# Kernel tuning notes

Measured on AMD Instinct MI355X. Metric: run time of the kernel, lower is better.

Reference implementation:

```python
import jax, jax.numpy as jnp
import numpy as np

N, E, FD, PD, C0, C1 = 50000, 1000000, 1024, 64, 64, 64


def setup_inputs() -> dict:
    key = jax.random.key(0)
    ks = iter(jax.random.split(key, 64))
    nrm = lambda s, sc=0.05: jax.random.normal(next(ks), s, jnp.float32) * sc

    def bn_p(c):
        # rows: gamma, beta, running_mean, running_var (eval-mode batchnorm)
        return jnp.stack([
            1.0 + 0.1 * jax.random.normal(next(ks), (c,)),
            0.1 * jax.random.normal(next(ks), (c,)),
            0.1 * jax.random.normal(next(ks), (c,)),
            0.5 + jax.random.uniform(next(ks), (c,)),
        ]).astype(jnp.float32)

    inp = {}
    inp["x"] = jax.random.normal(next(ks), (N, FD + 4), jnp.float32)
    inp["edge_index"] = jax.random.randint(next(ks), (2, E), 0, N, jnp.int32)
    inp["edge_attr"] = jax.random.randint(next(ks), (E,), 0, 3, jnp.int32) - 1  # {-1,0,1}
    inp["Wspf"] = nrm((PD, 4)); inp["bspf"] = nrm((PD,))
    inp["W011"] = nrm((C0, FD // 2 + PD)); inp["b011"] = nrm((C0,))
    inp["W012"] = nrm((C0, FD // 2)); inp["b012"] = nrm((C0,))
    inp["bn01"] = bn_p(C0)
    for i in (1, 2, 3):
        inp[f"e{i}W1"] = nrm((C0, 2 * C0)); inp[f"e{i}b1"] = nrm((C0,))
        inp[f"e{i}W2"] = nrm((C0, C0)); inp[f"e{i}b2"] = nrm((C0,))
        inp[f"bn1{i}"] = bn_p(C0)
    inp["s21Wl"] = nrm((C1, C0)); inp["s21bl"] = nrm((C1,)); inp["s21Wr"] = nrm((C1, C0))
    inp["bn21"] = bn_p(C1)
    for i in (1, 2, 3):
        inp[f"s3{i}Wl"] = nrm((1, C1)); inp[f"s3{i}bl"] = nrm((1,)); inp[f"s3{i}Wr"] = nrm((1, C1))
    return inp


def _bn(h, p):
    g, b, m, v = p
    return (h - m) * jax.lax.rsqrt(v + 1e-5) * g + b


def _edge_conv(h, src, dst, seg, n, W1, b1, W2, b2):
    # EdgeConv: max_j MLP([x_i, x_j - x_i]); masked edges routed to dummy segment n
    xi, xj = h[dst], h[src]
    msg = jax.nn.relu(jnp.concatenate([xi, xj - xi], axis=1) @ W1.T + b1) @ W2.T + b2
    out = jax.ops.segment_max(msg, seg, num_segments=n + 1)[:n]
    return jnp.where(jnp.isfinite(out), out, 0.0)  # nodes with no in-edges -> 0


def _sage(h, src, seg, n, Wl, bl, Wr):
    # SAGEConv: lin_l(mean_j x_j) + lin_r(x_i)
    s = jax.ops.segment_sum(h[src], seg, num_segments=n + 1)[:n]
    cnt = jax.ops.segment_sum(jnp.ones((seg.shape[0],), h.dtype), seg, num_segments=n + 1)[:n]
    agg = s / jnp.maximum(cnt, 1.0)[:, None]
    return agg @ Wl.T + bl + h @ Wr.T


def reference(x, edge_index, edge_attr, Wspf, bspf, W011, b011, W012, b012, bn01,
              e1W1, e1b1, e1W2, e1b2, bn11, e2W1, e2b1, e2W2, e2b2, bn12,
              e3W1, e3b1, e3W2, e3b2, bn13, s21Wl, s21bl, s21Wr, bn21,
              s31Wl, s31bl, s31Wr, s32Wl, s32bl, s32Wr, s33Wl, s33bl, s33Wr):
    fd = 1024
    n = x.shape[0]
    src, dst = edge_index[0], edge_index[1]
    seg1 = jnp.where(edge_attr >= 0, dst, n)  # forward-time edges
    seg2 = jnp.where(edge_attr <= 0, dst, n)  # backward-time edges
    seg3 = dst                                 # all edges

    spf = x[:, fd:fd + 4]
    x_vis = jnp.concatenate([x[:, fd // 2:fd], spf @ Wspf.T + bspf], axis=1) @ W011.T + b011
    x_aud = x[:, :fd // 2] @ W012.T + b012
    h = jax.nn.relu(_bn(x_aud + x_vis, bn01))

    def branch(eW1, eb1, eW2, eb2, bnE, seg, sWl, sbl, sWr):
        y = jax.nn.relu(_bn(_edge_conv(h, src, dst, seg, n, eW1, eb1, eW2, eb2), bnE))
        y = jax.nn.relu(_bn(_sage(y, src, seg, n, s21Wl, s21bl, s21Wr), bn21))
        return _sage(y, src, seg, n, sWl, sbl, sWr)

    o = (branch(e1W1, e1b1, e1W2, e1b2, bn11, seg1, s31Wl, s31bl, s31Wr)
         + branch(e2W1, e2b1, e2W2, e2b2, bn12, seg2, s32Wl, s32bl, s32Wr)
         + branch(e3W1, e3b1, e3W2, e3b2, bn13, seg3, s33Wl, s33bl, s33Wr))
    return jax.nn.sigmoid(o)
```

## Files before the change

### kernel.cpp

```cpp
#include <hip/hip_runtime.h>
#include <cstdint>
#include <cstddef>

#define NN 50000
#define EE 1000000
#define NBK 196
#define PWAVES 5120

typedef __attribute__((ext_vector_type(8))) short bf16x8;
typedef __attribute__((ext_vector_type(4))) short s16x4;
typedef __attribute__((ext_vector_type(4))) float f32x4;
typedef _Float16 f16;
typedef __attribute__((ext_vector_type(2))) _Float16 f16x2;
typedef __attribute__((ext_vector_type(4))) _Float16 f16x4;
typedef __attribute__((ext_vector_type(8))) _Float16 f16x8;

__device__ __forceinline__ unsigned short f2bf(float f) {
    union { unsigned int i; float f; } v; v.f = f;
    unsigned int u = v.i;
    u = u + 0x7FFFu + ((u >> 16) & 1u);
    return (unsigned short)(u >> 16);
}

__device__ __forceinline__ void split2(float v, short& hi, short& lo) {
    union { float f; unsigned int u; } a; a.f = v;
    unsigned short h16 = (unsigned short)(a.u >> 16);
    union { unsigned int u; float f; } hf; hf.u = ((unsigned int)h16) << 16;
    union { float f; unsigned int u; } b; b.f = v - hf.f;
    hi = (short)h16;
    lo = (short)(b.u >> 16);
}

#define OFF_WHL    ((size_t)0)
#define OFF_WSPP   ((size_t)262144)
#define OFF_BIAS01 ((size_t)263168)
#define OFF_W1PQT  ((size_t)263424)
#define OFF_BIASPQ ((size_t)361728)
#define OFF_WSAGET ((size_t)363264)
#define OFF_BIAS21 ((size_t)396032)
#define OFF_BNF    ((size_t)396288)
#define OFF_W2BF   ((size_t)398848)
#define OFF_INVC4  ((size_t)423424)
#define OFF_PZ4    ((size_t)1223424)
#define OFF_RP     ((size_t)2023424)
#define OFF_PARTS  ((size_t)2223488)
#define OFF_DEG    ((size_t)2227584)
#define OFF_GHEAD  ((size_t)2427648)
#define OFF_SORT   ((size_t)2431744)
#define OFF_H      ((size_t)6431744)
#define OFF_PI     ((size_t)19231744)
#define OFF_QI     ((size_t)38431744)
#define OFF_Y1I    ((size_t)57631744)
#define OFF_EBUCK  OFF_H
#define OFF_AGGI   OFF_PI

__global__ __launch_bounds__(256) void k_prep(
    const float* __restrict__ Wspf, const float* __restrict__ bspf,
    const float* __restrict__ W011, const float* __restrict__ b011,
    const float* __restrict__ W012, const float* __restrict__ b012,
    const float* __restrict__ bn01,
    const float* __restrict__ e1W1, const float* __restrict__ e1b1,
    const float* __restrict__ e1b2, const float* __restrict__ bn11,
    const float* __restrict__ e2W1, const float* __restrict__ e2b1,
    const float* __restrict__ e2b2, const float* __restrict__ bn12,
    const float* __restrict__ e3W1, const float* __restrict__ e3b1,
    const float* __restrict__ e3b2, const float* __restrict__ bn13,
    const float* __restrict__ e1W2, const float* __restrict__ e2W2,
    const float* __restrict__ e3W2,
    const float* __restrict__ s21Wl, const float* __restrict__ s21bl,
    const float* __restrict__ s21Wr, const float* __restrict__ bn21,
    unsigned short* __restrict__ Whl, float* __restrict__ WspP, float* __restrict__ bias01,
    float* __restrict__ W1pqT, float* __restrict__ biasPQ,
    float* __restrict__ WsageT, float* __restrict__ bias21, float* __restrict__ bnf,
    f16* __restrict__ W2h)
{
    int idx = blockIdx.x * 256 + threadIdx.x;
    if (idx < 131072) {
        int hl = idx >> 16;
        int r = idx & 65535;
        int kchunk = r >> 11;
        int r2 = r & 2047;
        int blk = r2 >> 9;
        int r3 = r2 & 511;
        int lane = r3 >> 3;
        int j = r3 & 7;
        int n = lane & 15, quad = lane >> 4;
        int k = kchunk * 32 + quad * 8 + j;
        int c = blk * 16 + n;
        float s = bn01[c] * rsqrtf(bn01[192 + c] + 1e-5f);
        float w = ((k < 512) ? W012[c * 512 + k] : W011[c * 576 + (k - 512)]) * s;
        short hi, lo;
        split2(w, hi, lo);
        Whl[idx] = (unsigned short)(hl ? lo : hi);
    } else if (idx < 131072 + 24576) {
        int r = idx - 131072;
        int b = r >> 13; r &= 8191;
        int k = r >> 7, cp = r & 127;
        const float* W1 = (b == 0) ? e1W1 : (b == 1) ? e2W1 : e3W1;
        float val;
        if (cp < 64) val = W1[cp * 128 + k] - W1[cp * 128 + 64 + k];
        else         val = W1[(cp - 64) * 128 + 64 + k];
        W1pqT[b * 8192 + k * 128 + cp] = val;
    } else if (idx < 131072 + 24576 + 8192) {
        int r = idx - (131072 + 24576);
        int k = r >> 6, c = r & 63;
        float s = bn21[c] * rsqrtf(bn21[192 + c] + 1e-5f);
        float w = (k < 64) ? s21Wl[c * 64 + k] : s21Wr[c * 64 + (k - 64)];
        WsageT[k * 64 + c] = w * s;
    } else if (idx < 131072 + 24576 + 8192 + 64) {
        int c = idx - (131072 + 24576 + 8192);
        float s01 = bn01[c] * rsqrtf(bn01[192 + c] + 1e-5f);
        float wsp0 = 0.f, wsp1 = 0.f, wsp2 = 0.f, wsp3 = 0.f, bacc = 0.f;
        for (int j = 0; j < 64; j++) {
            float w = W011[c * 576 + 512 + j];
            wsp0 += w * Wspf[j * 4 + 0];
            wsp1 += w * Wspf[j * 4 + 1];
            wsp2 += w * Wspf[j * 4 + 2];
            wsp3 += w * Wspf[j * 4 + 3];
            bacc += w * bspf[j];
        }
        WspP[c * 4 + 0] = wsp0 * s01; WspP[c * 4 + 1] = wsp1 * s01;
        WspP[c * 4 + 2] = wsp2 * s01; WspP[c * 4 + 3] = wsp3 * s01;
        bias01[c] = (b011[c] + b012[c] + bacc) * s01 + (bn01[64 + c] - bn01[128 + c] * s01);
        float s21 = bn21[c] * rsqrtf(bn21[192 + c] + 1e-5f);
        bias21[c] = s21bl[c] * s21 + (bn21[64 + c] - bn21[128 + c] * s21);
        const float* b1a[3] = { e1b1, e2b1, e3b1 };
        const float* b2a[3] = { e1b2, e2b2, e3b2 };
        const float* bna[3] = { bn11, bn12, bn13 };
#pragma unroll
        for (int b = 0; b < 3; b++) {
            float s = bna[b][c] * rsqrtf(bna[b][192 + c] + 1e-5f);
            float tr = bna[b][64 + c] - bna[b][128 + c] * s;
            bnf[b * 192 + c] = s;
            bnf[b * 192 + 64 + c] = b2a[b][c] * s + tr;
            bnf[b * 192 + 128 + c] = tr;
            biasPQ[b * 128 + c] = b1a[b][c];
            biasPQ[b * 128 + 64 + c] = 0.f;
        }
    } else if (idx < 131072 + 24576 + 8192 + 64 + 12288) {
        int r = idx - (131072 + 24576 + 8192 + 64);
        int b = r >> 12, i = r & 4095;
        const float* W2 = (b == 0) ? e1W2 : (b == 1) ? e2W2 : e3W2;
        W2h[b * 4096 + i] = (f16)W2[i];
    }
}

__global__ __launch_bounds__(256) void k_hist(
    const int* __restrict__ dst, int* __restrict__ deg)
{
    int e = blockIdx.x * 256 + threadIdx.x;
    if (e < EE) atomicAdd(&deg[dst[e]], 1);
}

__global__ __launch_bounds__(256) void k_psum(const int* __restrict__ deg, int* __restrict__ parts)
{
    int i = blockIdx.x * 256 + threadIdx.x;
    int v = (i < NN) ? deg[i] : 0;
#pragma unroll
    for (int off = 32; off > 0; off >>= 1) v += __shfl_xor(v, off);
    __shared__ int ws4[4];
    int wid = threadIdx.x >> 6;
    if ((threadIdx.x & 63) == 0) ws4[wid] = v;
    __syncthreads();
    if (threadIdx.x == 0)
        parts[blockIdx.x] = ws4[0] + ws4[1] + ws4[2] + ws4[3];
}

__global__ __launch_bounds__(256) void k_pscan(int* __restrict__ parts)
{
    __shared__ int sbuf[256];
    int tid = threadIdx.x;
    int v = (tid < NBK) ? parts[tid] : 0;
    sbuf[tid] = v;
    __syncthreads();
    for (int off = 1; off < 256; off <<= 1) {
        int t = (tid >= off) ? sbuf[tid - off] : 0;
        __syncthreads();
        sbuf[tid] += t;
        __syncthreads();
    }
    if (tid < NBK) parts[tid] = sbuf[tid] - v;
}

__global__ __launch_bounds__(256) void k_scanfix(
    const int* __restrict__ deg, const int* __restrict__ parts, int* __restrict__ rowptr)
{
    __shared__ int sbuf[256];
    int tid = threadIdx.x;
    int i = blockIdx.x * 256 + tid;
    int v = (i < NN) ? deg[i] : 0;
    sbuf[tid] = v;
    __syncthreads();
    for (int off = 1; off < 256; off <<= 1) {
        int t = (tid >= off) ? sbuf[tid - off] : 0;
        __syncthreads();
        sbuf[tid] += t;
        __syncthreads();
    }
    int base = parts[blockIdx.x];
    if (i < NN)      rowptr[i] = base + sbuf[tid] - v;
    if (i == NN - 1) rowptr[NN] = base + sbuf[tid];
}

__global__ __launch_bounds__(256) void k_gheadinit(
    const int* __restrict__ rp, int* __restrict__ ghead)
{
    int t = threadIdx.x;
    if (t < NBK) ghead[t] = rp[t * 256];
}

__global__ __launch_bounds__(256) void k_bucketA(
    const int* __restrict__ src, const int* __restrict__ dst, const int* __restrict__ attr,
    int* __restrict__ ghead, unsigned int* __restrict__ ebuck)
{
    __shared__ int hist[NBK];
    __shared__ int head[NBK];
    int tid = threadIdx.x;
    if (tid < NBK) hist[tid] = 0;
    __syncthreads();
    int base_e = blockIdx.x * 4096;
    unsigned int word[16]; int bkt[16];
#pragma unroll
    for (int k = 0; k < 16; k++) {
        int e = base_e + k * 256 + tid;
        if (e < EE) {
            int d = dst[e], s = src[e], a = attr[e] + 1;
            int b = d >> 8;
            word[k] = (unsigned)s | ((unsigned)a << 16) | ((unsigned)(d & 255) << 18);
            bkt[k] = b;
            atomicAdd(&hist[b], 1);
        } else { bkt[k] = -1; word[k] = 0; }
    }
    __syncthreads();
    if (tid < NBK) {
        int c = hist[tid];
        head[tid] = c ? atomicAdd(&ghead[tid], c) : 0;
    }
    __syncthreads();
#pragma unroll
    for (int k = 0; k < 16; k++) {
        if (bkt[k] >= 0) {
            int pos = atomicAdd(&head[bkt[k]], 1);
            ebuck[pos] = word[k];
        }
    }
}

__global__ __launch_bounds__(256) void k_bucketB(
    const int* __restrict__ rp, const unsigned int* __restrict__ ebuck,
    int* __restrict__ sorted)
{
    __shared__ int sbuf[256];
    __shared__ int head[256];
    int b = blockIdx.x, tid = threadIdx.x;
    int n0 = b * 256;
    int n1 = n0 + 256; if (n1 > NN) n1 = NN;
    int r0 = rp[n0];
    int r1 = rp[n1];
    sbuf[tid] = 0;
    __syncthreads();
    for (int e = r0 + tid; e < r1; e += 256)
        atomicAdd(&sbuf[(ebuck[e] >> 18) & 255], 1);
    __syncthreads();
    int v = sbuf[tid];
    for (int off = 1; off < 256; off <<= 1) {
        int t = (tid >= off) ? sbuf[tid - off] : 0;
        __syncthreads();
        sbuf[tid] += t;
        __syncthreads();
    }
    head[tid] = r0 + sbuf[tid] - v;
    __syncthreads();
    for (int e = r0 + tid; e < r1; e += 256) {
        unsigned int w = ebuck[e];
        int pos = atomicAdd(&head[(w >> 18) & 255], 1);
        sorted[pos] = (int)(w & 0x3FFFFu);
    }
}

__global__ __launch_bounds__(256) void k_h(
    const float* __restrict__ x, const unsigned short* __restrict__ Whl,
    const float* __restrict__ WspP, const float* __restrict__ bias01,
    float* __restrict__ h)
{
    __shared__ unsigned short hib[2][4096];
    __shared__ unsigned short lob[2][4096];
    int tid = threadIdx.x;
    int w = tid >> 6, l = tid & 63;
    int tile = blockIdx.x;
    int m = l & 15, quad = l >> 4;
    int blk = w;
    const unsigned short* Wh = Whl;
    const unsigned short* Wl = Whl + 65536;
    const size_t xbase = (size_t)tile * 16 * 1028;

    int oct_w = l >> 1, off_w = (l & 1) * 4;

    f32x4 g[4];
#pragma unroll
    for (int p = 0; p < 4; p++)
        g[p] = *(const f32x4*)(x + xbase + (size_t)(p * 4 + w) * 1028 + l * 4);
#pragma unroll
    for (int p = 0; p < 4; p++) {
        int r = p * 4 + w;
        int op = r * 256 + (oct_w ^ (r & 7)) * 8 + off_w;
        s16x4 h4, l4;
#pragma unroll
        for (int i = 0; i < 4; i++) { short hi, lo; split2(g[p][i], hi, lo); h4[i] = hi; l4[i] = lo; }
        *(s16x4*)(&hib[0][op]) = h4;
        *(s16x4*)(&lob[0][op]) = l4;
    }
    __syncthreads();

    f32x4 acc = { 0.f, 0.f, 0.f, 0.f };
    for (int c = 0; c < 4; c++) {
        if (c < 3) {
#pragma unroll
            for (int p = 0; p < 4; p++)
                g[p] = *(const f32x4*)(x + xbase + (size_t)(p * 4 + w) * 1028 + (c + 1) * 256 + l * 4);
        }
        int buf = c & 1;
        const unsigned short* hp = &hib[buf][m * 256];
        const unsigned short* lp = &lob[buf][m * 256];
        int msw = m & 7;
#pragma unroll
        for (int ks = 0; ks < 8; ks++) {
            int oct = ks * 4 + quad;
            int ao = (oct ^ msw) * 8;
            bf16x8 xh = *(const bf16x8*)(hp + ao);
            bf16x8 xl = *(const bf16x8*)(lp + ao);
            int fb = (c * 8 + ks) * 2048 + blk * 512 + l * 8;
            bf16x8 bh = *(const bf16x8*)(Wh + fb);
            bf16x8 bl = *(const bf16x8*)(Wl + fb);
            acc = __builtin_amdgcn_mfma_f32_16x16x32_bf16(xh, bh, acc, 0, 0, 0);
            acc = __builtin_amdgcn_mfma_f32_16x16x32_bf16(xl, bh, acc, 0, 0, 0);
            acc = __builtin_amdgcn_mfma_f32_16x16x32_bf16(xh, bl, acc, 0, 0, 0);
        }
        if (c < 3) {
            int nbuf = (c + 1) & 1;
#pragma unroll
            for (int p = 0; p < 4; p++) {
                int r = p * 4 + w;
                int op = r * 256 + (oct_w ^ (r & 7)) * 8 + off_w;
                s16x4 h4, l4;
#pragma unroll
                for (int i = 0; i < 4; i++) { short hi, lo; split2(g[p][i], hi, lo); h4[i] = hi; l4[i] = lo; }
                *(s16x4*)(&hib[nbuf][op]) = h4;
                *(s16x4*)(&lob[nbuf][op]) = l4;
            }
            __syncthreads();
        }
    }

    int ch = blk * 16 + m;
    f32x4 wsp = *(const f32x4*)(WspP + ch * 4);
    float bia = bias01[ch];
#pragma unroll
    for (int r = 0; r < 4; r++) {
        int row = tile * 16 + quad * 4 + r;
        f32x4 sp = *(const f32x4*)(x + (size_t)row * 1028 + 1024);
        float a = acc[r] + sp[0] * wsp[0] + sp[1] * wsp[1]
                + sp[2] * wsp[2] + sp[3] * wsp[3] + bia;
        h[(size_t)row * 64 + ch] = fmaxf(a, 0.f);
    }
}

__global__ __launch_bounds__(256) void k_pq(
    const float* __restrict__ h, const float* __restrict__ WT,
    const float* __restrict__ biasP, f16* __restrict__ Pi, f16* __restrict__ Qi)
{
    __shared__ float wt[64 * 128];
    __shared__ float xt[64 * 68];
    int tid = threadIdx.x;
    int m0 = blockIdx.x * 64;
    int cg = tid & 31, rg = tid >> 5;
#pragma unroll
    for (int i = 0; i < 8; i++)
        ((float4*)wt)[i * 256 + tid] = ((const float4*)WT)[i * 256 + tid];
#pragma unroll
    for (int i = 0; i < 4; i++) {
        int li = i * 256 + tid;
        int rr = li >> 4, q = li & 15;
        int row = m0 + rr;
        float4 u = make_float4(0.f, 0.f, 0.f, 0.f);
        if (row < NN) u = *(const float4*)(h + (size_t)row * 64 + q * 4);
        *(float4*)(xt + rr * 68 + q * 4) = u;
    }
    __syncthreads();
    float acc[8][4];
#pragma unroll
    for (int r = 0; r < 8; r++)
#pragma unroll
        for (int j = 0; j < 4; j++) acc[r][j] = 0.f;
#pragma unroll 8
    for (int k = 0; k < 64; k++) {
        float4 wv = *(const float4*)(wt + k * 128 + cg * 4);
#pragma unroll
        for (int r = 0; r < 8; r++) {
            float xv = xt[(rg * 8 + r) * 68 + k];
            acc[r][0] += xv * wv.x; acc[r][1] += xv * wv.y;
            acc[r][2] += xv * wv.z; acc[r][3] += xv * wv.w;
        }
    }
#pragma unroll
    for (int r = 0; r < 8; r++) {
        int row = m0 + rg * 8 + r;
        if (row < NN) {
            if (cg < 16) {
                f16x4 res;
#pragma unroll
                for (int j = 0; j < 4; j++)
                    res[j] = (f16)(acc[r][j] + biasP[cg * 4 + j]);
                *(f16x4*)(Pi + (size_t)row * 192 + cg * 4) = res;
            } else {
                f16x4 res;
#pragma unroll
                for (int j = 0; j < 4; j++)
                    res[j] = (f16)acc[r][j];
                *(f16x4*)(Qi + (size_t)row * 192 + (cg - 16) * 4) = res;
            }
        }
    }
}

#define ECV_LDS_BRANCH(B, PL, PH, Q0, Q1, MASK, ACC)                               \
    if ((MASK) & 0xFFFFull) {                                                      \
        f16x8 a0, a1;                                                              \
        _Pragma("unroll") for (int j = 0; j < 8; j++) {                            \
            f16 s0 = PL[j] + Q0[j]; a0[j] = (s0 > (f16)0.f) ? s0 : (f16)0.f;       \
            f16 s1 = PH[j] + Q1[j]; a1[j] = (s1 > (f16)0.f) ? s1 : (f16)0.f;       \
        }                                                                          \
        _Pragma("unroll") for (int blk = 0; blk < 4; blk++) {                      \
            f32x4 c = { 0.f, 0.f, 0.f, 0.f };                                      \
            f16x8 w0 = *(const f16x8*)(w2s + ((B) * 8 + blk * 2 + 0) * 512 + quad * 128 + m * 8); \
            f16x8 w1 = *(const f16x8*)(w2s + ((B) * 8 + blk * 2 + 1) * 512 + quad * 128 + m * 8); \
            c = __builtin_amdgcn_mfma_f32_16x16x32_f16(a0, w0, c, 0, 0, 0);        \
            c = __builtin_amdgcn_mfma_f32_16x16x32_f16(a1, w1, c, 0, 0, 0);        \
            _Pragma("unroll") for (int r = 0; r < 4; r++)                          \
                if (((MASK) >> (vsh + r)) & 1)                                     \
                    ACC[blk][r] = fmaxf(ACC[blk][r], c[r]);                        \
        }                                                                          \
    }

#define ECV_EPI(B, ACC, CNT)                                                       \
    {                                                                              \
        float red[4];                                                              \
        _Pragma("unroll") for (int blk = 0; blk < 4; blk++) {                      \
            float rv = fmaxf(fmaxf(ACC[blk][0], ACC[blk][1]),                      \
                             fmaxf(ACC[blk][2], ACC[blk][3]));                     \
            rv = fmaxf(rv, __shfl_xor(rv, 16));                                    \
            rv = fmaxf(rv, __shfl_xor(rv, 32));                                    \
            red[blk] = rv;                                                         \
        }                                                                          \
        float mx = red[quad];                                                      \
        const float* scb = bnf + (B) * 192;                                        \
        float outv = ((CNT) > 0) ? fmaxf(fmaf(mx, scb[lane], scb[64 + lane]), 0.f) \
                                 : fmaxf(scb[128 + lane], 0.f);                    \
        y1i[(size_t)v * 192 + (B) * 64 + lane] = (f16)outv;                        \
    }

__global__ __launch_bounds__(256) void k_edgeconv_f(
    const int* __restrict__ rowptr, const int* __restrict__ sorted,
    const f16* __restrict__ Pi, const f16* __restrict__ Qi,
    const f16* __restrict__ W2h,
    const float* __restrict__ bnf,
    f16* __restrict__ y1i, float* __restrict__ invc4)
{
    __shared__ f16 w2s[8192];
    int tid = threadIdx.x;
#pragma unroll
    for (int u0 = 0; u0 < 4; u0++) {
        int u = u0 * 256 + tid;
        int frag = u >> 6;
        int rem = u & 63;
        int m2 = rem >> 2, qd = rem & 3;
        int bb = frag >> 3, blk = (frag >> 1) & 3, kc = frag & 1;
        *(int4*)(w2s + frag * 512 + qd * 128 + m2 * 8) =
            *(const int4*)(W2h + (bb * 64 + blk * 16 + m2) * 64 + kc * 32 + qd * 8);
    }
    __syncthreads();

    int wid = tid >> 6, lane = tid & 63;
    int m = lane & 15, quad = lane >> 4;
    int gw = blockIdx.x * 4 + wid;

    f16x8 wf3[4][2];
#pragma unroll
    for (int blk = 0; blk < 4; blk++)
#pragma unroll
        for (int kc = 0; kc < 2; kc++)
            wf3[blk][kc] = *(const f16x8*)(W2h + 2 * 4096 + (blk * 16 + m) * 64 + kc * 32 + quad * 8);

    for (int v = gw; v < NN; v += PWAVES) {
        const f16* pr = Pi + (size_t)v * 192;
        f16x8 pl0 = *(const f16x8*)(pr + 0   + quad * 8);
        f16x8 ph0 = *(const f16x8*)(pr + 32  + quad * 8);
        f16x8 pl1 = *(const f16x8*)(pr + 64  + quad * 8);
        f16x8 ph1 = *(const f16x8*)(pr + 96  + quad * 8);
        f16x8 pl2 = *(const f16x8*)(pr + 128 + quad * 8);
        f16x8 ph2 = *(const f16x8*)(pr + 160 + quad * 8);

        int e0 = rowptr[v], e1 = rowptr[v + 1];
        int deg = e1 - e0;
        float acc0[4][4], acc1[4][4], acc2[4][4];
#pragma unroll
        for (int blk = 0; blk < 4; blk++)
#pragma unroll
            for (int r = 0; r < 4; r++) {
                acc0[blk][r] = -3.0e38f; acc1[blk][r] = -3.0e38f; acc2[blk][r] = -3.0e38f;
            }

        int cnt1 = 0, cnt2 = 0;
        int nb = (deg + 15) >> 4;
        for (int bi = 0; bi < nb; bi++) {
            int e = e0 + bi * 16 + m;
            bool in = e < e1;
            int wrd = in ? sorted[e] : 0;
            int srcm = in ? (wrd & 0xFFFF) : v;
            int a = (wrd >> 16) & 3;
            bool mm1 = in && (a >= 1);
            bool mm2 = in && (a <= 1);
            const f16* qr = Qi + (size_t)srcm * 192;
            f16x8 q30 = *(const f16x8*)(qr + 128 + quad * 8);
            f16x8 q31 = *(const f16x8*)(qr + 160 + quad * 8);
            f16x8 q10 = {}, q11 = {}, q20 = {}, q21 = {};
            if (mm1) { q10 = *(const f16x8*)(qr + quad * 8);      q11 = *(const f16x8*)(qr + 32 + quad * 8); }
            if (mm2) { q20 = *(const f16x8*)(qr + 64 + quad * 8); q21 = *(const f16x8*)(qr + 96 + quad * 8); }
            unsigned long long bl1 = __ballot(mm1);
            unsigned long long bl2 = __ballot(mm2);
            unsigned long long bl3 = __ballot(in);
            cnt1 += __popc((unsigned)bl1 & 0xFFFFu);
            cnt2 += __popc((unsigned)bl2 & 0xFFFFu);
            int vsh = quad * 4;

            {
                f16x8 a0, a1;
#pragma unroll
                for (int j = 0; j < 8; j++) {
                    f16 s0 = pl2[j] + q30[j]; a0[j] = (s0 > (f16)0.f) ? s0 : (f16)0.f;
                    f16 s1 = ph2[j] + q31[j]; a1[j] = (s1 > (f16)0.f) ? s1 : (f16)0.f;
                }
#pragma unroll
                for (int blk = 0; blk < 4; blk++) {
                    f32x4 c = { 0.f, 0.f, 0.f, 0.f };
                    c = __builtin_amdgcn_mfma_f32_16x16x32_f16(a0, wf3[blk][0], c, 0, 0, 0);
                    c = __builtin_amdgcn_mfma_f32_16x16x32_f16(a1, wf3[blk][1], c, 0, 0, 0);
#pragma unroll
                    for (int r = 0; r < 4; r++)
                        if ((bl3 >> (vsh + r)) & 1)
                            acc2[blk][r] = fmaxf(acc2[blk][r], c[r]);
                }
            }
            ECV_LDS_BRANCH(0, pl0, ph0, q10, q11, bl1, acc0)
            ECV_LDS_BRANCH(1, pl1, ph1, q20, q21, bl2, acc1)
        }

        ECV_EPI(0, acc0, cnt1)
        ECV_EPI(1, acc1, cnt2)
        ECV_EPI(2, acc2, deg)
        if (lane == 0) {
            float4 ic;
            ic.x = 1.f / (float)(cnt1 > 0 ? cnt1 : 1);
            ic.y = 1.f / (float)(cnt2 > 0 ? cnt2 : 1);
            ic.z = 1.f / (float)(deg  > 0 ? deg  : 1);
            ic.w = 0.f;
            *(float4*)(invc4 + (size_t)v * 4) = ic;
        }
    }
}

__global__ __launch_bounds__(256) void k_agg_f(
    const int* __restrict__ rowptr, const int* __restrict__ sorted,
    const f16* __restrict__ y1i, const float* __restrict__ invc4,
    f16* __restrict__ aggi)
{
    int wid = threadIdx.x >> 6, lane = threadIdx.x & 63;
    int hf = lane >> 5, c = lane & 31;
    int gw = blockIdx.x * 4 + wid;
    for (int v = gw; v < NN; v += PWAVES) {
        int e0 = rowptr[v], e1 = rowptr[v + 1];
        float s1a = 0.f, s1b = 0.f, s2a = 0.f, s2b = 0.f, s3a = 0.f, s3b = 0.f;
        float t1a = 0.f, t1b = 0.f, t2a = 0.f, t2b = 0.f, t3a = 0.f, t3b = 0.f;
        int e = e0;
        for (; e + 4 <= e1; e += 4) {
            int wA = sorted[e + hf];
            int wB = sorted[e + 2 + hf];
            {
                int src = wA & 0xFFFF, a = (wA >> 16) & 3;
                const f16* row = y1i + (size_t)src * 192 + c * 2;
                f16x2 u3 = *(const f16x2*)(row + 128); s3a += (float)u3[0]; s3b += (float)u3[1];
                if (a >= 1) { f16x2 u = *(const f16x2*)(row);      s1a += (float)u[0]; s1b += (float)u[1]; }
                if (a <= 1) { f16x2 u = *(const f16x2*)(row + 64); s2a += (float)u[0]; s2b += (float)u[1]; }
            }
            {
                int src = wB & 0xFFFF, a = (wB >> 16) & 3;
                const f16* row = y1i + (size_t)src * 192 + c * 2;
                f16x2 u3 = *(const f16x2*)(row + 128); t3a += (float)u3[0]; t3b += (float)u3[1];
                if (a >= 1) { f16x2 u = *(const f16x2*)(row);      t1a += (float)u[0]; t1b += (float)u[1]; }
                if (a <= 1) { f16x2 u = *(const f16x2*)(row + 64); t2a += (float)u[0]; t2b += (float)u[1]; }
            }
        }
        for (; e + 2 <= e1; e += 2) {
            int wA = sorted[e + hf];
            int src = wA & 0xFFFF, a = (wA >> 16) & 3;
            const f16* row = y1i + (size_t)src * 192 + c * 2;
            f16x2 u3 = *(const f16x2*)(row + 128); s3a += (float)u3[0]; s3b += (float)u3[1];
            if (a >= 1) { f16x2 u = *(const f16x2*)(row);      s1a += (float)u[0]; s1b += (float)u[1]; }
            if (a <= 1) { f16x2 u = *(const f16x2*)(row + 64); s2a += (float)u[0]; s2b += (float)u[1]; }
        }
        if (e < e1 && hf == 0) {
            int wA = sorted[e];
            int src = wA & 0xFFFF, a = (wA >> 16) & 3;
            const f16* row = y1i + (size_t)src * 192 + c * 2;
            f16x2 u3 = *(const f16x2*)(row + 128); s3a += (float)u3[0]; s3b += (float)u3[1];
            if (a >= 1) { f16x2 u = *(const f16x2*)(row);      s1a += (float)u[0]; s1b += (float)u[1]; }
            if (a <= 1) { f16x2 u = *(const f16x2*)(row + 64); s2a += (float)u[0]; s2b += (float)u[1]; }
        }
        s1a += t1a; s1b += t1b; s2a += t2a; s2b += t2b; s3a += t3a; s3b += t3b;
        s1a += __shfl_xor(s1a, 32); s1b += __shfl_xor(s1b, 32);
        s2a += __shfl_xor(s2a, 32); s2b += __shfl_xor(s2b, 32);
        s3a += __shfl_xor(s3a, 32); s3b += __shfl_xor(s3b, 32);
        if (hf == 0) {
            float4 icv = *(const float4*)(invc4 + (size_t)v * 4);
            f16* od = aggi + (size_t)v * 192 + c * 2;
            f16x2 r1; r1[0] = (f16)(s1a * icv.x); r1[1] = (f16)(s1b * icv.x); *(f16x2*)(od)       = r1;
            f16x2 r2; r2[0] = (f16)(s2a * icv.y); r2[1] = (f16)(s2b * icv.y); *(f16x2*)(od + 64)  = r2;
            f16x2 r3; r3[0] = (f16)(s3a * icv.z); r3[1] = (f16)(s3b * icv.z); *(f16x2*)(od + 128) = r3;
        }
    }
}

__global__ __launch_bounds__(256) void k_sage1(
    const f16* __restrict__ aggA, const f16* __restrict__ y1A,
    const float* __restrict__ WsageT, const float* __restrict__ bias21,
    const float* __restrict__ Wl3, const float* __restrict__ bl3,
    const float* __restrict__ Wr3,
    float* __restrict__ pz4, int b)
{
    __shared__ float wt[64 * 64];
    __shared__ float xt[128 * 68];
    __shared__ float wl[64], wr[64];
    int tid = threadIdx.x;
    int m0 = blockIdx.x * 128;
    int cg = tid & 15, rg = tid >> 4;
    if (tid < 64) { wl[tid] = Wl3[tid]; wr[tid] = Wr3[tid]; }
    float blv = bl3[0];
    float acc[8][4];
#pragma unroll
    for (int r = 0; r < 8; r++)
#pragma unroll
        for (int j = 0; j < 4; j++) acc[r][j] = 0.f;
    for (int ch = 0; ch < 2; ch++) {
        const f16* A = ch ? y1A : aggA;
        __syncthreads();
#pragma unroll
        for (int i = 0; i < 4; i++)
            ((float4*)wt)[i * 256 + tid] = ((const float4*)(WsageT + ch * 4096))[i * 256 + tid];
#pragma unroll
        for (int i = 0; i < 4; i++) {
            int li = i * 256 + tid;
            int rr = li >> 3, q = li & 7;
            int row = m0 + rr;
            f16x8 u = {};
            if (row < NN) u = *(const f16x8*)(A + (size_t)row * 192 + q * 8);
            float4 lo4 = make_float4((float)u[0], (float)u[1], (float)u[2], (float)u[3]);
            float4 hi4 = make_float4((float)u[4], (float)u[5], (float)u[6], (float)u[7]);
            *(float4*)(xt + rr * 68 + q * 8) = lo4;
            *(float4*)(xt + rr * 68 + q * 8 + 4) = hi4;
        }
        __syncthreads();
#pragma unroll 8
        for (int k = 0; k < 64; k++) {
            float4 wv = *(const float4*)(wt + k * 64 + cg * 4);
#pragma unroll
            for (int r = 0; r < 8; r++) {
                float xv = xt[(rg * 8 + r) * 68 + k];
                acc[r][0] += xv * wv.x; acc[r][1] += xv * wv.y;
                acc[r][2] += xv * wv.z; acc[r][3] += xv * wv.w;
            }
        }
    }
#pragma unroll
    for (int r = 0; r < 8; r++) {
        int row = m0 + rg * 8 + r;
        float ap = 0.f, az = 0.f;
#pragma unroll
        for (int j = 0; j < 4; j++) {
            float t = fmaxf(acc[r][j] + bias21[cg * 4 + j], 0.f);
            ap += t * wl[cg * 4 + j];
            az += t * wr[cg * 4 + j];
        }
        ap += __shfl_xor(ap, 1); ap += __shfl_xor(ap, 2);
        ap += __shfl_xor(ap, 4); ap += __shfl_xor(ap, 8);
        az += __shfl_xor(az, 1); az += __shfl_xor(az, 2);
        az += __shfl_xor(az, 4); az += __shfl_xor(az, 8);
        if (cg == 0 && row < NN) {
            pz4[(size_t)row * 4 + b] = ap;
            float zz = az + blv;
            if (b == 0) pz4[(size_t)row * 4 + 3] = zz;
            else        pz4[(size_t)row * 4 + 3] += zz;
        }
    }
}

__global__ __launch_bounds__(256) void k_sage2_f(
    const int* __restrict__ rowptr, const int* __restrict__ sorted,
    const float* __restrict__ pz4, const float* __restrict__ invc4,
    float* __restrict__ outp)
{
    int wid = threadIdx.x >> 6, lane = threadIdx.x & 63;
    int gw = blockIdx.x * 4 + wid;
    for (int v = gw; v < NN; v += PWAVES) {
        int e0 = rowptr[v], e1 = rowptr[v + 1];
        float s1 = 0.f, s2 = 0.f, s3 = 0.f;
        for (int e = e0 + lane; e < e1; e += 64) {
            int w = sorted[e];
            int src = w & 0xFFFF, a = (w >> 16) & 3;
            float4 pz = *(const float4*)(pz4 + (size_t)src * 4);
            s3 += pz.z;
            if (a >= 1) s1 += pz.x;
            if (a <= 1) s2 += pz.y;
        }
#pragma unroll
        for (int off = 32; off > 0; off >>= 1) {
            s1 += __shfl_xor(s1, off);
            s2 += __shfl_xor(s2, off);
            s3 += __shfl_xor(s3, off);
        }
        if (lane == 0) {
            float4 icv = *(const float4*)(invc4 + (size_t)v * 4);
            float zsum = pz4[(size_t)v * 4 + 3];
            float val = s1 * icv.x + s2 * icv.y + s3 * icv.z + zsum;
            outp[v] = 1.f / (1.f + expf(-val));
        }
    }
}

extern "C" void kernel_launch(void* const* d_in, const int* in_sizes, int n_in,
                              void* d_out, int out_size, void* d_ws, size_t ws_size,
                              hipStream_t stream)
{
    const float* x    = (const float*)d_in[0];
    const int* ei     = (const int*)d_in[1];
    const int* attr   = (const int*)d_in[2];
    const float* Wspf = (const float*)d_in[3];
    const float* bspf = (const float*)d_in[4];
    const float* W011 = (const float*)d_in[5];
    const float* b011 = (const float*)d_in[6];
    const float* W012 = (const float*)d_in[7];
    const float* b012 = (const float*)d_in[8];
    const float* bn01 = (const float*)d_in[9];
    const float* eW1[3] = { (const float*)d_in[10], (const float*)d_in[15], (const float*)d_in[20] };
    const float* eb1[3] = { (const float*)d_in[11], (const float*)d_in[16], (const float*)d_in[21] };
    const float* eW2[3] = { (const float*)d_in[12], (const float*)d_in[17], (const float*)d_in[22] };
    const float* eb2[3] = { (const float*)d_in[13], (const float*)d_in[18], (const float*)d_in[23] };
    const float* bn1[3] = { (const float*)d_in[14], (const float*)d_in[19], (const float*)d_in[24] };
    const float* s21Wl = (const float*)d_in[25];
    const float* s21bl = (const float*)d_in[26];
    const float* s21Wr = (const float*)d_in[27];
    const float* bn21  = (const float*)d_in[28];
    const float* s3Wl[3] = { (const float*)d_in[29], (const float*)d_in[32], (const float*)d_in[35] };
    const float* s3bl[3] = { (const float*)d_in[30], (const float*)d_in[33], (const float*)d_in[36] };
    const float* s3Wr[3] = { (const float*)d_in[31], (const float*)d_in[34], (const float*)d_in[37] };

    char* ws = (char*)d_ws;
    unsigned short* Whl = (unsigned short*)(ws + OFF_WHL);
    float* WspP   = (float*)(ws + OFF_WSPP);
    float* bias01 = (float*)(ws + OFF_BIAS01);
    float* W1pqT  = (float*)(ws + OFF_W1PQT);
    float* biasPQ = (float*)(ws + OFF_BIASPQ);
    float* WsageT = (float*)(ws + OFF_WSAGET);
    float* bias21 = (float*)(ws + OFF_BIAS21);
    float* bnf    = (float*)(ws + OFF_BNF);
    f16*   W2h    = (f16*)(ws + OFF_W2BF);
    float* invc4  = (float*)(ws + OFF_INVC4);
    float* pz4    = (float*)(ws + OFF_PZ4);
    int*   rp     = (int*)(ws + OFF_RP);
    int*   parts  = (int*)(ws + OFF_PARTS);
    int*   deg    = (int*)(ws + OFF_DEG);
    int*   ghead  = (int*)(ws + OFF_GHEAD);
    int*   sorted = (int*)(ws + OFF_SORT);
    unsigned int* ebuck = (unsigned int*)(ws + OFF_EBUCK);
    float* h      = (float*)(ws + OFF_H);
    f16*   Pi     = (f16*)(ws + OFF_PI);
    f16*   Qi     = (f16*)(ws + OFF_QI);
    f16*   y1i    = (f16*)(ws + OFF_Y1I);
    f16*   aggi   = (f16*)(ws + OFF_AGGI);

    hipMemsetAsync(ws + OFF_DEG, 0, 200064, stream);

    k_prep<<<689, 256, 0, stream>>>(
        Wspf, bspf, W011, b011, W012, b012, bn01,
        eW1[0], eb1[0], eb2[0], bn1[0],
        eW1[1], eb1[1], eb2[1], bn1[1],
        eW1[2], eb1[2], eb2[2], bn1[2],
        eW2[0], eW2[1], eW2[2],
        s21Wl, s21bl, s21Wr, bn21,
        Whl, WspP, bias01, W1pqT, biasPQ, WsageT, bias21, bnf, W2h);

    k_hist<<<3907, 256, 0, stream>>>(ei + EE, deg);
    k_psum<<<NBK, 256, 0, stream>>>(deg, parts);
    k_pscan<<<1, 256, 0, stream>>>(parts);
    k_scanfix<<<NBK, 256, 0, stream>>>(deg, parts, rp);
    k_gheadinit<<<1, 256, 0, stream>>>(rp, ghead);
    k_bucketA<<<245, 256, 0, stream>>>(ei, ei + EE, attr, ghead, ebuck);
    k_bucketB<<<NBK, 256, 0, stream>>>(rp, ebuck, sorted);

    k_h<<<3125, 256, 0, stream>>>(x, Whl, WspP, bias01, h);

    for (int b = 0; b < 3; b++)
        k_pq<<<782, 256, 0, stream>>>(h, W1pqT + b * 8192, biasPQ + b * 128,
                                      Pi + b * 64, Qi + b * 64);

    k_edgeconv_f<<<PWAVES / 4, 256, 0, stream>>>(rp, sorted, Pi, Qi, W2h, bnf, y1i, invc4);
    k_agg_f<<<PWAVES / 4, 256, 0, stream>>>(rp, sorted, y1i, invc4, aggi);

    for (int b = 0; b < 3; b++)
        k_sage1<<<391, 256, 0, stream>>>(aggi + b * 64, y1i + b * 64, WsageT, bias21,
                                         s3Wl[b], s3bl[b], s3Wr[b], pz4, b);

    k_sage2_f<<<PWAVES / 4, 256, 0, stream>>>(rp, sorted, pz4, invc4, (float*)d_out);
}
```

Baseline: 846.5 us.

## Merge PQ launches, split edgeconv full/tail blocks, widen agg gathers

```diff
diff --git a/kernel.cpp b/kernel.cpp
--- a/kernel.cpp
+++ b/kernel.cpp
@@ -15,13 +15,6 @@
 typedef __attribute__((ext_vector_type(4))) _Float16 f16x4;
 typedef __attribute__((ext_vector_type(8))) _Float16 f16x8;
 
-__device__ __forceinline__ unsigned short f2bf(float f) {
-    union { unsigned int i; float f; } v; v.f = f;
-    unsigned int u = v.i;
-    u = u + 0x7FFFu + ((u >> 16) & 1u);
-    return (unsigned short)(u >> 16);
-}
-
 __device__ __forceinline__ void split2(float v, short& hi, short& lo) {
     union { float f; unsigned int u; } a; a.f = v;
     unsigned short h16 = (unsigned short)(a.u >> 16);
@@ -29,6 +22,19 @@
     union { float f; unsigned int u; } b; b.f = v - hf.f;
     hi = (short)h16;
     lo = (short)(b.u >> 16);
+}
+
+__device__ __forceinline__ f16x8 relupq(f16x8 p, f16x8 q) {
+    f16x8 s = p + q;
+    f16x8 z = {};
+#if __has_builtin(__builtin_elementwise_max)
+    return __builtin_elementwise_max(s, z);
+#else
+    f16x8 r;
+#pragma unroll
+    for (int j = 0; j < 8; j++) r[j] = (s[j] > (f16)0.f) ? s[j] : (f16)0.f;
+    return r;
+#endif
 }
 
 #define OFF_WHL    ((size_t)0)
@@ -366,17 +372,14 @@
 }
 
 __global__ __launch_bounds__(256) void k_pq(
-    const float* __restrict__ h, const float* __restrict__ WT,
-    const float* __restrict__ biasP, f16* __restrict__ Pi, f16* __restrict__ Qi)
+    const float* __restrict__ h, const float* __restrict__ WT3,
+    const float* __restrict__ biasPQ, f16* __restrict__ Pi, f16* __restrict__ Qi)
 {
     __shared__ float wt[64 * 128];
     __shared__ float xt[64 * 68];
     int tid = threadIdx.x;
     int m0 = blockIdx.x * 64;
     int cg = tid & 31, rg = tid >> 5;
-#pragma unroll
-    for (int i = 0; i < 8; i++)
-        ((float4*)wt)[i * 256 + tid] = ((const float4*)WT)[i * 256 + tid];
 #pragma unroll
     for (int i = 0; i < 4; i++) {
         int li = i * 256 + tid;
@@ -386,59 +389,60 @@
         if (row < NN) u = *(const float4*)(h + (size_t)row * 64 + q * 4);
         *(float4*)(xt + rr * 68 + q * 4) = u;
     }
-    __syncthreads();
-    float acc[8][4];
-#pragma unroll
-    for (int r = 0; r < 8; r++)
-#pragma unroll
-        for (int j = 0; j < 4; j++) acc[r][j] = 0.f;
+    for (int b = 0; b < 3; b++) {
+        __syncthreads();
+#pragma unroll
+        for (int i = 0; i < 8; i++)
+            ((float4*)wt)[i * 256 + tid] = ((const float4*)(WT3 + b * 8192))[i * 256 + tid];
+        __syncthreads();
+        float acc[8][4];
+#pragma unroll
+        for (int r = 0; r < 8; r++)
+#pragma unroll
+            for (int j = 0; j < 4; j++) acc[r][j] = 0.f;
 #pragma unroll 8
-    for (int k = 0; k < 64; k++) {
-        float4 wv = *(const float4*)(wt + k * 128 + cg * 4);
+        for (int k = 0; k < 64; k++) {
+            float4 wv = *(const float4*)(wt + k * 128 + cg * 4);
+#pragma unroll
+            for (int r = 0; r < 8; r++) {
+                float xv = xt[(rg * 8 + r) * 68 + k];
+                acc[r][0] += xv * wv.x; acc[r][1] += xv * wv.y;
+                acc[r][2] += xv * wv.z; acc[r][3] += xv * wv.w;
+            }
+        }
+        const float* biasP = biasPQ + b * 128;
 #pragma unroll
         for (int r = 0; r < 8; r++) {
-            float xv = xt[(rg * 8 + r) * 68 + k];
-            acc[r][0] += xv * wv.x; acc[r][1] += xv * wv.y;
-            acc[r][2] += xv * wv.z; acc[r][3] += xv * wv.w;
-        }
-    }
-#pragma unroll
-    for (int r = 0; r < 8; r++) {
-        int row = m0 + rg * 8 + r;
-        if (row < NN) {
-            if (cg < 16) {
-                f16x4 res;
-#pragma unroll
-                for (int j = 0; j < 4; j++)
-                    res[j] = (f16)(acc[r][j] + biasP[cg * 4 + j]);
-                *(f16x4*)(Pi + (size_t)row * 192 + cg * 4) = res;
-            } else {
-                f16x4 res;
-#pragma unroll
-                for (int j = 0; j < 4; j++)
-                    res[j] = (f16)acc[r][j];
-                *(f16x4*)(Qi + (size_t)row * 192 + (cg - 16) * 4) = res;
-            }
-        }
-    }
-}
-
-#define ECV_LDS_BRANCH(B, PL, PH, Q0, Q1, MASK, ACC)                               \
-    if ((MASK) & 0xFFFFull) {                                                      \
-        f16x8 a0, a1;                                                              \
-        _Pragma("unroll") for (int j = 0; j < 8; j++) {                            \
-            f16 s0 = PL[j] + Q0[j]; a0[j] = (s0 > (f16)0.f) ? s0 : (f16)0.f;       \
-            f16 s1 = PH[j] + Q1[j]; a1[j] = (s1 > (f16)0.f) ? s1 : (f16)0.f;       \
-        }                                                                          \
+            int row = m0 + rg * 8 + r;
+            if (row < NN) {
+                if (cg < 16) {
+                    f16x4 res;
+#pragma unroll
+                    for (int j = 0; j < 4; j++)
+                        res[j] = (f16)(acc[r][j] + biasP[cg * 4 + j]);
+                    *(f16x4*)(Pi + (size_t)row * 192 + b * 64 + cg * 4) = res;
+                } else {
+                    f16x4 res;
+#pragma unroll
+                    for (int j = 0; j < 4; j++)
+                        res[j] = (f16)acc[r][j];
+                    *(f16x4*)(Qi + (size_t)row * 192 + b * 64 + (cg - 16) * 4) = res;
+                }
+            }
+        }
+    }
+}
+
+#define ECV_BR_LDS(B, AF0, AF1, AM, ACC)                                           \
+    {                                                                              \
         _Pragma("unroll") for (int blk = 0; blk < 4; blk++) {                      \
             f32x4 c = { 0.f, 0.f, 0.f, 0.f };                                      \
             f16x8 w0 = *(const f16x8*)(w2s + ((B) * 8 + blk * 2 + 0) * 512 + quad * 128 + m * 8); \
             f16x8 w1 = *(const f16x8*)(w2s + ((B) * 8 + blk * 2 + 1) * 512 + quad * 128 + m * 8); \
-            c = __builtin_amdgcn_mfma_f32_16x16x32_f16(a0, w0, c, 0, 0, 0);        \
-            c = __builtin_amdgcn_mfma_f32_16x16x32_f16(a1, w1, c, 0, 0, 0);        \
+            c = __builtin_amdgcn_mfma_f32_16x16x32_f16(AF0, w0, c, 0, 0, 0);       \
+            c = __builtin_amdgcn_mfma_f32_16x16x32_f16(AF1, w1, c, 0, 0, 0);       \
             _Pragma("unroll") for (int r = 0; r < 4; r++)                          \
-                if (((MASK) >> (vsh + r)) & 1)                                     \
-                    ACC[blk][r] = fmaxf(ACC[blk][r], c[r]);                        \
+                ACC[blk][r] = fmaxf(ACC[blk][r], c[r] + AM[r]);                    \
         }                                                                          \
     }
 
@@ -511,9 +515,58 @@
             }
 
         int cnt1 = 0, cnt2 = 0;
-        int nb = (deg + 15) >> 4;
-        for (int bi = 0; bi < nb; bi++) {
+        int vsh = quad * 4;
+        int nbf = deg >> 4;
+
+        for (int bi = 0; bi < nbf; bi++) {
             int e = e0 + bi * 16 + m;
+            int wrd = sorted[e];
+            int srcm = wrd & 0xFFFF;
+            int a = (wrd >> 16) & 3;
+            const f16* qr = Qi + (size_t)srcm * 192;
+            f16x8 q10 = *(const f16x8*)(qr + 0   + quad * 8);
+            f16x8 q11 = *(const f16x8*)(qr + 32  + quad * 8);
+            f16x8 q20 = *(const f16x8*)(qr + 64  + quad * 8);
+            f16x8 q21 = *(const f16x8*)(qr + 96  + quad * 8);
+            f16x8 q30 = *(const f16x8*)(qr + 128 + quad * 8);
+            f16x8 q31 = *(const f16x8*)(qr + 160 + quad * 8);
+            unsigned long long bl1 = __ballot(a >= 1);
+            unsigned long long bl2 = __ballot(a <= 1);
+            cnt1 += __popc((unsigned)bl1 & 0xFFFFu);
+            cnt2 += __popc((unsigned)bl2 & 0xFFFFu);
+            float am1[4], am2[4];
+#pragma unroll
+            for (int r = 0; r < 4; r++) {
+                am1[r] = ((bl1 >> (vsh + r)) & 1) ? 0.f : -3.0e38f;
+                am2[r] = ((bl2 >> (vsh + r)) & 1) ? 0.f : -3.0e38f;
+            }
+            {
+                f16x8 a0 = relupq(pl2, q30);
+                f16x8 a1 = relupq(ph2, q31);
+#pragma unroll
+                for (int blk = 0; blk < 4; blk++) {
+                    f32x4 c = { 0.f, 0.f, 0.f, 0.f };
+                    c = __builtin_amdgcn_mfma_f32_16x16x32_f16(a0, wf3[blk][0], c, 0, 0, 0);
+                    c = __builtin_amdgcn_mfma_f32_16x16x32_f16(a1, wf3[blk][1], c, 0, 0, 0);
+#pragma unroll
+                    for (int r = 0; r < 4; r++)
+                        acc2[blk][r] = fmaxf(acc2[blk][r], c[r]);
+                }
+            }
+            {
+                f16x8 a0 = relupq(pl0, q10);
+                f16x8 a1 = relupq(ph0, q11);
+                ECV_BR_LDS(0, a0, a1, am1, acc0)
+            }
+            {
+                f16x8 a0 = relupq(pl1, q20);
+                f16x8 a1 = relupq(ph1, q21);
+                ECV_BR_LDS(1, a0, a1, am2, acc1)
+            }
+        }
+
+        if (deg & 15) {
+            int e = e0 + nbf * 16 + m;
             bool in = e < e1;
             int wrd = in ? sorted[e] : 0;
             int srcm = in ? (wrd & 0xFFFF) : v;
@@ -521,25 +574,27 @@
             bool mm1 = in && (a >= 1);
             bool mm2 = in && (a <= 1);
             const f16* qr = Qi + (size_t)srcm * 192;
+            f16x8 q10 = *(const f16x8*)(qr + 0   + quad * 8);
+            f16x8 q11 = *(const f16x8*)(qr + 32  + quad * 8);
+            f16x8 q20 = *(const f16x8*)(qr + 64  + quad * 8);
+            f16x8 q21 = *(const f16x8*)(qr + 96  + quad * 8);
             f16x8 q30 = *(const f16x8*)(qr + 128 + quad * 8);
             f16x8 q31 = *(const f16x8*)(qr + 160 + quad * 8);
-            f16x8 q10 = {}, q11 = {}, q20 = {}, q21 = {};
-            if (mm1) { q10 = *(const f16x8*)(qr + quad * 8);      q11 = *(const f16x8*)(qr + 32 + quad * 8); }
-            if (mm2) { q20 = *(const f16x8*)(qr + 64 + quad * 8); q21 = *(const f16x8*)(qr + 96 + quad * 8); }
             unsigned long long bl1 = __ballot(mm1);
             unsigned long long bl2 = __ballot(mm2);
             unsigned long long bl3 = __ballot(in);
             cnt1 += __popc((unsigned)bl1 & 0xFFFFu);
             cnt2 += __popc((unsigned)bl2 & 0xFFFFu);
-            int vsh = quad * 4;
-
+            float am1[4], am2[4], am3[4];
+#pragma unroll
+            for (int r = 0; r < 4; r++) {
+                am1[r] = ((bl1 >> (vsh + r)) & 1) ? 0.f : -3.0e38f;
+                am2[r] = ((bl2 >> (vsh + r)) & 1) ? 0.f : -3.0e38f;
+                am3[r] = ((bl3 >> (vsh + r)) & 1) ? 0.f : -3.0e38f;
+            }
             {
-                f16x8 a0, a1;
-#pragma unroll
-                for (int j = 0; j < 8; j++) {
-                    f16 s0 = pl2[j] + q30[j]; a0[j] = (s0 > (f16)0.f) ? s0 : (f16)0.f;
-                    f16 s1 = ph2[j] + q31[j]; a1[j] = (s1 > (f16)0.f) ? s1 : (f16)0.f;
-                }
+                f16x8 a0 = relupq(pl2, q30);
+                f16x8 a1 = relupq(ph2, q31);
 #pragma unroll
                 for (int blk = 0; blk < 4; blk++) {
                     f32x4 c = { 0.f, 0.f, 0.f, 0.f };
@@ -547,12 +602,19 @@
                     c = __builtin_amdgcn_mfma_f32_16x16x32_f16(a1, wf3[blk][1], c, 0, 0, 0);
 #pragma unroll
                     for (int r = 0; r < 4; r++)
-                        if ((bl3 >> (vsh + r)) & 1)
-                            acc2[blk][r] = fmaxf(acc2[blk][r], c[r]);
+                        acc2[blk][r] = fmaxf(acc2[blk][r], c[r] + am3[r]);
                 }
             }
-            ECV_LDS_BRANCH(0, pl0, ph0, q10, q11, bl1, acc0)
-            ECV_LDS_BRANCH(1, pl1, ph1, q20, q21, bl2, acc1)
+            if (bl1 & 0xFFFFull) {
+                f16x8 a0 = relupq(pl0, q10);
+                f16x8 a1 = relupq(ph0, q11);
+                ECV_BR_LDS(0, a0, a1, am1, acc0)
+            }
+            if (bl2 & 0xFFFFull) {
+                f16x8 a0 = relupq(pl1, q20);
+                f16x8 a1 = relupq(ph1, q21);
+                ECV_BR_LDS(1, a0, a1, am2, acc1)
+            }
         }
 
         ECV_EPI(0, acc0, cnt1)
@@ -575,57 +637,52 @@
     f16* __restrict__ aggi)
 {
     int wid = threadIdx.x >> 6, lane = threadIdx.x & 63;
-    int hf = lane >> 5, c = lane & 31;
+    int eslot = lane >> 3, cg = lane & 7;
     int gw = blockIdx.x * 4 + wid;
     for (int v = gw; v < NN; v += PWAVES) {
         int e0 = rowptr[v], e1 = rowptr[v + 1];
-        float s1a = 0.f, s1b = 0.f, s2a = 0.f, s2b = 0.f, s3a = 0.f, s3b = 0.f;
-        float t1a = 0.f, t1b = 0.f, t2a = 0.f, t2b = 0.f, t3a = 0.f, t3b = 0.f;
-        int e = e0;
-        for (; e + 4 <= e1; e += 4) {
-            int wA = sorted[e + hf];
-            int wB = sorted[e + 2 + hf];
-            {
-                int src = wA & 0xFFFF, a = (wA >> 16) & 3;
-                const f16* row = y1i + (size_t)src * 192 + c * 2;
-                f16x2 u3 = *(const f16x2*)(row + 128); s3a += (float)u3[0]; s3b += (float)u3[1];
-                if (a >= 1) { f16x2 u = *(const f16x2*)(row);      s1a += (float)u[0]; s1b += (float)u[1]; }
-                if (a <= 1) { f16x2 u = *(const f16x2*)(row + 64); s2a += (float)u[0]; s2b += (float)u[1]; }
-            }
-            {
-                int src = wB & 0xFFFF, a = (wB >> 16) & 3;
-                const f16* row = y1i + (size_t)src * 192 + c * 2;
-                f16x2 u3 = *(const f16x2*)(row + 128); t3a += (float)u3[0]; t3b += (float)u3[1];
-                if (a >= 1) { f16x2 u = *(const f16x2*)(row);      t1a += (float)u[0]; t1b += (float)u[1]; }
-                if (a <= 1) { f16x2 u = *(const f16x2*)(row + 64); t2a += (float)u[0]; t2b += (float)u[1]; }
-            }
-        }
-        for (; e + 2 <= e1; e += 2) {
-            int wA = sorted[e + hf];
-            int src = wA & 0xFFFF, a = (wA >> 16) & 3;
-            const f16* row = y1i + (size_t)src * 192 + c * 2;
-            f16x2 u3 = *(const f16x2*)(row + 128); s3a += (float)u3[0]; s3b += (float)u3[1];
-            if (a >= 1) { f16x2 u = *(const f16x2*)(row);      s1a += (float)u[0]; s1b += (float)u[1]; }
-            if (a <= 1) { f16x2 u = *(const f16x2*)(row + 64); s2a += (float)u[0]; s2b += (float)u[1]; }
-        }
-        if (e < e1 && hf == 0) {
-            int wA = sorted[e];
-            int src = wA & 0xFFFF, a = (wA >> 16) & 3;
-            const f16* row = y1i + (size_t)src * 192 + c * 2;
-            f16x2 u3 = *(const f16x2*)(row + 128); s3a += (float)u3[0]; s3b += (float)u3[1];
-            if (a >= 1) { f16x2 u = *(const f16x2*)(row);      s1a += (float)u[0]; s1b += (float)u[1]; }
-            if (a <= 1) { f16x2 u = *(const f16x2*)(row + 64); s2a += (float)u[0]; s2b += (float)u[1]; }
-        }
-        s1a += t1a; s1b += t1b; s2a += t2a; s2b += t2b; s3a += t3a; s3b += t3b;
-        s1a += __shfl_xor(s1a, 32); s1b += __shfl_xor(s1b, 32);
-        s2a += __shfl_xor(s2a, 32); s2b += __shfl_xor(s2b, 32);
-        s3a += __shfl_xor(s3a, 32); s3b += __shfl_xor(s3b, 32);
-        if (hf == 0) {
+        float s1[8], s2[8], s3[8];
+#pragma unroll
+        for (int j = 0; j < 8; j++) { s1[j] = 0.f; s2[j] = 0.f; s3[j] = 0.f; }
+        for (int eb = e0; eb < e1; eb += 8) {
+            int e = eb + eslot;
+            bool val = e < e1;
+            int ec = val ? e : (e1 - 1);
+            int w = sorted[ec];
+            int src = w & 0xFFFF, a = (w >> 16) & 3;
+            float f3 = val ? 1.f : 0.f;
+            float f1 = (val && a >= 1) ? 1.f : 0.f;
+            float f2 = (val && a <= 1) ? 1.f : 0.f;
+            const f16* row = y1i + (size_t)src * 192 + cg * 8;
+            f16x8 u1 = *(const f16x8*)(row);
+            f16x8 u2 = *(const f16x8*)(row + 64);
+            f16x8 u3 = *(const f16x8*)(row + 128);
+#pragma unroll
+            for (int j = 0; j < 8; j++) {
+                s1[j] = fmaf(f1, (float)u1[j], s1[j]);
+                s2[j] = fmaf(f2, (float)u2[j], s2[j]);
+                s3[j] = fmaf(f3, (float)u3[j], s3[j]);
+            }
+        }
+#pragma unroll
+        for (int j = 0; j < 8; j++) {
+            s1[j] += __shfl_xor(s1[j], 8);  s1[j] += __shfl_xor(s1[j], 16); s1[j] += __shfl_xor(s1[j], 32);
+            s2[j] += __shfl_xor(s2[j], 8);  s2[j] += __shfl_xor(s2[j], 16); s2[j] += __shfl_xor(s2[j], 32);
+            s3[j] += __shfl_xor(s3[j], 8);  s3[j] += __shfl_xor(s3[j], 16); s3[j] += __shfl_xor(s3[j], 32);
+        }
+        if (eslot == 0) {
             float4 icv = *(const float4*)(invc4 + (size_t)v * 4);
-            f16* od = aggi + (size_t)v * 192 + c * 2;
-            f16x2 r1; r1[0] = (f16)(s1a * icv.x); r1[1] = (f16)(s1b * icv.x); *(f16x2*)(od)       = r1;
-            f16x2 r2; r2[0] = (f16)(s2a * icv.y); r2[1] = (f16)(s2b * icv.y); *(f16x2*)(od + 64)  = r2;
-            f16x2 r3; r3[0] = (f16)(s3a * icv.z); r3[1] = (f16)(s3b * icv.z); *(f16x2*)(od + 128) = r3;
+            f16* od = aggi + (size_t)v * 192 + cg * 8;
+            f16x8 r1, r2, r3;
+#pragma unroll
+            for (int j = 0; j < 8; j++) {
+                r1[j] = (f16)(s1[j] * icv.x);
+                r2[j] = (f16)(s2[j] * icv.y);
+                r3[j] = (f16)(s3[j] * icv.z);
+            }
+            *(f16x8*)(od)       = r1;
+            *(f16x8*)(od + 64)  = r2;
+            *(f16x8*)(od + 128) = r3;
         }
     }
 }
@@ -808,9 +865,7 @@
 
     k_h<<<3125, 256, 0, stream>>>(x, Whl, WspP, bias01, h);
 
-    for (int b = 0; b < 3; b++)
-        k_pq<<<782, 256, 0, stream>>>(h, W1pqT + b * 8192, biasPQ + b * 128,
-                                      Pi + b * 64, Qi + b * 64);
+    k_pq<<<782, 256, 0, stream>>>(h, W1pqT, biasPQ, Pi, Qi);
 
     k_edgeconv_f<<<PWAVES / 4, 256, 0, stream>>>(rp, sorted, Pi, Qi, W2h, bnf, y1i, invc4);
     k_agg_f<<<PWAVES / 4, 256, 0, stream>>>(rp, sorted, y1i, invc4, aggi);
```

Result: slower. 873.7 us (+3.2%).
